# Kernel tuning notes

Measured on AMD Instinct MI355X. Metric: run time of the kernel, lower is better.

## Reference

```python
import jax, jax.numpy as jnp
import numpy as np

B, S, F, D, VOCAB, H = 1024, 512, 4, 32, 100001, 64
LN_EPS = 1e-3  # keras LayerNormalization default


def setup_inputs() -> dict:
    key = jax.random.key(0)
    ks = jax.random.split(key, 16)
    sd = 0.05
    return {
        "values": jax.random.normal(ks[0], (B, S, F), jnp.float32),
        "names": jax.random.randint(ks[1], (B, S), 0, VOCAB),
        "emb_table": jax.random.normal(ks[2], (VOCAB, D), jnp.float32) * sd,
        "W_num": jax.random.normal(ks[3], (F, D), jnp.float32) * sd,
        "b_num": jnp.zeros((D,), jnp.float32),
        "Wq": jax.random.normal(ks[4], (D, D), jnp.float32) * sd,
        "bq": jnp.zeros((D,), jnp.float32),
        "Wv": jax.random.normal(ks[5], (D, D), jnp.float32) * sd,
        "bv": jnp.zeros((D,), jnp.float32),
        "attn_scale": jnp.ones((D,), jnp.float32),
        "Wp": jax.random.normal(ks[6], (D, H), jnp.float32) * sd,
        "bp": jnp.zeros((H,), jnp.float32),
        "ln_gamma": jnp.ones((H,), jnp.float32),
        "ln_beta": jnp.zeros((H,), jnp.float32),
        "Ws": jax.random.normal(ks[7], (H, 2), jnp.float32) * sd,
    }


def reference(values, names, emb_table, W_num, b_num, Wq, bq, Wv, bv,
              attn_scale, Wp, bp, ln_gamma, ln_beta, Ws):
    # embeddings + numerical projection  [B,S,D]
    v = values @ W_num + b_num
    e = emb_table[names]
    mix = e + v
    # query from last position, value/key from the rest
    q = mix[:, -1:, :] @ Wq + bq          # [B,1,D]
    val = mix[:, :-1, :] @ Wv + bv        # [B,S-1,D]
    # keras AdditiveAttention (use_scale=True): score = sum(scale*tanh(q+k))
    scores = jnp.sum(attn_scale * jnp.tanh(q[:, :, None, :] + val[:, None, :, :]), axis=-1)  # [B,1,S-1]
    attn = jax.nn.softmax(scores, axis=-1)
    emb_out = jnp.einsum('bij,bjd->bid', attn, val)  # [B,1,D]
    # broadcast add then mean over sequence
    context = jnp.mean(emb_out + mix, axis=1)        # [B,D]
    # predictor: Dense(relu) + LayerNorm(axis=1 == features)
    h = jax.nn.relu(context @ Wp + bp)               # [B,H]
    mu = jnp.mean(h, axis=1, keepdims=True)
    var = jnp.var(h, axis=1, keepdims=True)
    h = (h - mu) * jax.lax.rsqrt(var + LN_EPS) * ln_gamma + ln_beta
    # scorer: Dense(2, softmax, no bias)
    score = jax.nn.softmax(h @ Ws, axis=-1)          # [B,2]
    return (score, emb_out, attn, h)
```

## Files before the change

kernel.cpp:

```cpp
#include <hip/hip_runtime.h>
#include <hip/hip_bf16.h>
#include <math.h>

constexpr int Bsz   = 1024;
constexpr int S     = 512;
constexpr int SV    = 511;
constexpr int D     = 32;
constexpr int F     = 4;
constexpr int H     = 64;
constexpr int BDIM  = 256;
constexpr int VOCAB = 100001;
constexpr size_t TAB_BYTES = (size_t)VOCAB * 64 * 2;

__device__ __forceinline__ float fast_tanh(float x) {
  const float ex = __expf(2.f * x);
  return 1.f - 2.f * __builtin_amdgcn_rcpf(ex + 1.f);
}

__device__ __forceinline__ void unpack8(uint4 u, float* f) {
  f[0] = __uint_as_float(u.x << 16); f[1] = __uint_as_float(u.x & 0xffff0000u);
  f[2] = __uint_as_float(u.y << 16); f[3] = __uint_as_float(u.y & 0xffff0000u);
  f[4] = __uint_as_float(u.z << 16); f[5] = __uint_as_float(u.z & 0xffff0000u);
  f[6] = __uint_as_float(u.w << 16); f[7] = __uint_as_float(u.w & 0xffff0000u);
}

__global__ __launch_bounds__(BDIM) void build_tab(
    const float* __restrict__ emb, const float* __restrict__ Wv,
    const float* __restrict__ W_num, const float* __restrict__ b_num,
    const float* __restrict__ bv,
    __hip_bfloat16* __restrict__ T, float* __restrict__ wsc)
{
  __shared__ float sWv[D * D];
  for (int i = threadIdx.x; i < D * D; i += BDIM) sWv[i] = Wv[i];
  __syncthreads();

  if (blockIdx.x == gridDim.x - 1) {
    const int tid = threadIdx.x;
    if (tid < F * D) {
      const int f = tid >> 5, k = tid & 31;
      float a = 0.f;
      #pragma unroll
      for (int m = 0; m < D; m++) a += W_num[f * D + m] * sWv[m * D + k];
      wsc[k * 4 + f] = a;
    } else if (tid < F * D + D) {
      const int k = tid - F * D;
      float a = bv[k];
      #pragma unroll
      for (int m = 0; m < D; m++) a += b_num[m] * sWv[m * D + k];
      wsc[F * D + k] = a;
    }
    return;
  }

  const int lr = threadIdx.x >> 5, k = threadIdx.x & 31;
  const int row = blockIdx.x * 8 + lr;
  if (row < VOCAB) {
    const float4* e4 = reinterpret_cast<const float4*>(emb + (size_t)row * D);
    float a = 0.f;
    #pragma unroll
    for (int c = 0; c < 8; c++) {
      const float4 v = e4[c];
      a += v.x * sWv[(4 * c + 0) * D + k] + v.y * sWv[(4 * c + 1) * D + k]
         + v.z * sWv[(4 * c + 2) * D + k] + v.w * sWv[(4 * c + 3) * D + k];
    }
    T[(size_t)row * 64 + k]      = __float2bfloat16(emb[(size_t)row * D + k]);
    T[(size_t)row * 64 + 32 + k] = __float2bfloat16(a);
  }
}

__global__ __launch_bounds__(BDIM, 4) void attn_main(
    const float* __restrict__ values, const int* __restrict__ names,
    const __hip_bfloat16* __restrict__ T, const float* __restrict__ wsc,
    const float* __restrict__ emb,
    const float* __restrict__ W_num, const float* __restrict__ b_num,
    const float* __restrict__ Wq,    const float* __restrict__ bq,
    const float* __restrict__ attn_scale,
    const float* __restrict__ Wp,    const float* __restrict__ bp,
    const float* __restrict__ ln_g,  const float* __restrict__ ln_b,
    const float* __restrict__ Ws,
    float* __restrict__ out_score, float* __restrict__ out_emb,
    float* __restrict__ out_attn,  float* __restrict__ out_h)
{
  __shared__ float sW2T[D][4];
  __shared__ float sQS[D][2];
  __shared__ float smixq[D];
  __shared__ float sred[4][69];
  __shared__ float sctx[D];
  __shared__ float sL[1];
  __shared__ float sE[512];

  const int b = blockIdx.x, tid = threadIdx.x, lane = tid & 63, wv = tid >> 6;
  const int rg = lane >> 2, kl = lane & 3;
  const int rbase = wv * 16 + rg;

  if (tid < 128) sW2T[tid >> 2][tid & 3] = wsc[tid];
  if (tid < D) {
    const int    nq = names[b * S + (S - 1)];
    const float* vr = values + (size_t)(b * S + (S - 1)) * F;
    smixq[tid] = emb[(size_t)nq * D + tid] + b_num[tid]
               + vr[0] * W_num[tid] + vr[1] * W_num[D + tid]
               + vr[2] * W_num[2 * D + tid] + vr[3] * W_num[3 * D + tid];
  }
  __syncthreads();
  if (tid < D) {
    float a = bq[tid];
    #pragma unroll
    for (int m = 0; m < D; m++) a += smixq[m] * Wq[m * D + tid];
    sQS[tid][0] = a + wsc[128 + tid];
    sQS[tid][1] = attn_scale[tid];
  }
  __syncthreads();

  float qb[8], scl[8], w2a[8], w2b[8], w2c[8], w2d[8];
  #pragma unroll
  for (int i = 0; i < 8; i++) {
    const int k = kl * 8 + i;
    qb[i]  = sQS[k][0]; scl[i] = sQS[k][1];
    w2a[i] = sW2T[k][0]; w2b[i] = sW2T[k][1];
    w2c[i] = sW2T[k][2]; w2d[i] = sW2T[k][3];
  }

  int nm[8];
  #pragma unroll
  for (int p = 0; p < 8; p++) nm[p] = names[b * S + p * 64 + rbase];

  float esum[8], acc[8];
  #pragma unroll
  for (int i = 0; i < 8; i++) { esum[i] = 0.f; acc[i] = 0.f; }
  float lloc = 0.f, vs0 = 0.f, vs1 = 0.f, vs2 = 0.f, vs3 = 0.f;

  const char* Tb = (const char*)T;
  uint4 Ec, Wc, En, Wn; float4 vc, vn;
  {
    const char* p0 = Tb + (size_t)nm[0] * 128 + kl * 16;
    Ec = *(const uint4*)p0; Wc = *(const uint4*)(p0 + 64);
    vc = *reinterpret_cast<const float4*>(values + (size_t)(b * S + rbase) * F);
    const char* p1 = Tb + (size_t)nm[1] * 128 + kl * 16;
    En = *(const uint4*)p1; Wn = *(const uint4*)(p1 + 64);
    vn = *reinterpret_cast<const float4*>(values + (size_t)(b * S + 64 + rbase) * F);
  }

  #pragma unroll
  for (int p = 0; p < 8; p++) {
    float em[8], w[8], t[8];
    unpack8(Ec, em); unpack8(Wc, w);
    float s = 0.f;
    #pragma unroll
    for (int i = 0; i < 8; i++) {
      t[i] = w[i] + qb[i] + vc.x * w2a[i] + vc.y * w2b[i]
           + vc.z * w2c[i] + vc.w * w2d[i];
      s += scl[i] * fast_tanh(t[i]);
    }
    const float4 vcur = vc;
    Ec = En; Wc = Wn; vc = vn;
    if (p + 2 < 8) {
      const char* pn = Tb + (size_t)nm[p + 2] * 128 + kl * 16;
      En = *(const uint4*)pn; Wn = *(const uint4*)(pn + 64);
      vn = *reinterpret_cast<const float4*>(values + (size_t)(b * S + (p + 2) * 64 + rbase) * F);
    }
    s += __shfl_xor(s, 1); s += __shfl_xor(s, 2);
    const bool  valid = (p * 64 + rbase) < SV;
    const float e = valid ? __expf(s) : 0.f;
    lloc += e;
    if (kl == 0) sE[p * 64 + rbase] = e;
    if (valid) {
      vs0 += vcur.x; vs1 += vcur.y; vs2 += vcur.z; vs3 += vcur.w;
      #pragma unroll
      for (int i = 0; i < 8; i++) esum[i] += em[i];
    }
    #pragma unroll
    for (int i = 0; i < 8; i++) acc[i] = fmaf(e, t[i], acc[i]);
  }

  #pragma unroll
  for (int off = 4; off < 64; off <<= 1) {
    lloc += __shfl_xor(lloc, off);
    vs0 += __shfl_xor(vs0, off); vs1 += __shfl_xor(vs1, off);
    vs2 += __shfl_xor(vs2, off); vs3 += __shfl_xor(vs3, off);
    #pragma unroll
    for (int i = 0; i < 8; i++) {
      acc[i]  += __shfl_xor(acc[i], off);
      esum[i] += __shfl_xor(esum[i], off);
    }
  }
  if (lane < 4) {
    #pragma unroll
    for (int i = 0; i < 8; i++) {
      sred[wv][lane * 8 + i]      = acc[i];
      sred[wv][32 + lane * 8 + i] = esum[i];
    }
  }
  if (lane == 0) {
    sred[wv][64] = lloc;
    sred[wv][65] = vs0; sred[wv][66] = vs1; sred[wv][67] = vs2; sred[wv][68] = vs3;
  }
  __syncthreads();
  if (tid == 0) sL[0] = sred[0][64] + sred[1][64] + sred[2][64] + sred[3][64];
  __syncthreads();
  const float invL = 1.f / sL[0];

  for (int idx = tid; idx < SV; idx += BDIM)
    out_attn[(size_t)b * SV + idx] = sE[idx] * invL;

  if (tid < D) {
    const float aS = sred[0][tid] + sred[1][tid] + sred[2][tid] + sred[3][tid];
    const float eS = sred[0][D + tid] + sred[1][D + tid] + sred[2][D + tid] + sred[3][D + tid];
    float vp = 0.f;
    #pragma unroll
    for (int f = 0; f < 4; f++) {
      const float vf = sred[0][65 + f] + sred[1][65 + f] + sred[2][65 + f] + sred[3][65 + f];
      vp += vf * W_num[f * D + tid];
    }
    const float q  = sQS[tid][0] - wsc[128 + tid];
    const float eo = aS * invL - q;
    out_emb[(size_t)b * D + tid] = eo;
    sctx[tid] = eo + (eS + vp + (float)SV * b_num[tid] + smixq[tid]) * (1.f / (float)S);
  }
  __syncthreads();

  if (tid < H) {
    float hv = bp[tid];
    #pragma unroll
    for (int d = 0; d < D; d++) hv += sctx[d] * Wp[d * H + tid];
    hv = fmaxf(hv, 0.f);
    float mu = hv;
    #pragma unroll
    for (int off = 32; off; off >>= 1) mu += __shfl_xor(mu, off);
    mu *= (1.f / 64.f);
    const float dv = hv - mu;
    float vvv = dv * dv;
    #pragma unroll
    for (int off = 32; off; off >>= 1) vvv += __shfl_xor(vvv, off);
    vvv *= (1.f / 64.f);
    const float hn = dv * rsqrtf(vvv + 1e-3f) * ln_g[tid] + ln_b[tid];
    out_h[(size_t)b * H + tid] = hn;
    float s0 = hn * Ws[2 * tid], s1 = hn * Ws[2 * tid + 1];
    #pragma unroll
    for (int off = 32; off; off >>= 1) { s0 += __shfl_xor(s0, off); s1 += __shfl_xor(s1, off); }
    if (tid == 0) {
      const float mx = fmaxf(s0, s1);
      const float a0 = __expf(s0 - mx), a1 = __expf(s1 - mx);
      const float inv = 1.f / (a0 + a1);
      out_score[(size_t)b * 2]     = a0 * inv;
      out_score[(size_t)b * 2 + 1] = a1 * inv;
    }
  }
}

__global__ __launch_bounds__(BDIM) void attn_fused_gemv(
    const float* __restrict__ values, const int* __restrict__ names,
    const float* __restrict__ emb,
    const float* __restrict__ W_num, const float* __restrict__ b_num,
    const float* __restrict__ Wq,    const float* __restrict__ bq,
    const float* __restrict__ Wv,    const float* __restrict__ bv,
    const float* __restrict__ attn_scale,
    const float* __restrict__ Wp,    const float* __restrict__ bp,
    const float* __restrict__ ln_g,  const float* __restrict__ ln_b,
    const float* __restrict__ Ws,
    float* __restrict__ out_score, float* __restrict__ out_emb,
    float* __restrict__ out_attn,  float* __restrict__ out_h)
{
  __shared__ float sWnum[F * D];
  __shared__ float sbnum[D];
  __shared__ float sWq[D * D];
  __shared__ float sWv[D * D];
  __shared__ float sbv[D];
  __shared__ float sscale[D];
  __shared__ float sq[D];
  __shared__ float smixq[D];
  __shared__ float sred[4][2 * D];
  __shared__ float sredS[4];
  __shared__ float sML[2];
  __shared__ float sctx[D];
  __shared__ float sWp[D * H];

  const int b = blockIdx.x, tid = threadIdx.x, lane = tid & 63, wv = tid >> 6;

  for (int i = tid; i < F * D; i += BDIM) sWnum[i] = W_num[i];
  if (tid < D) { sbnum[tid] = b_num[tid]; sbv[tid] = bv[tid]; sscale[tid] = attn_scale[tid]; }
  for (int i = tid; i < D * D; i += BDIM) { sWq[i] = Wq[i]; sWv[i] = Wv[i]; }
  for (int i = tid; i < D * H; i += BDIM) sWp[i] = Wp[i];
  __syncthreads();

  if (tid < D) {
    const int    name = names[b * S + (S - 1)];
    const float* vr   = values + (size_t)(b * S + (S - 1)) * F;
    smixq[tid] = emb[(size_t)name * D + tid] + sbnum[tid]
               + vr[0] * sWnum[tid] + vr[1] * sWnum[D + tid]
               + vr[2] * sWnum[2 * D + tid] + vr[3] * sWnum[3 * D + tid];
  }
  __syncthreads();
  if (tid < D) {
    float a = bq[tid];
    #pragma unroll
    for (int k = 0; k < D; k++) a += smixq[k] * sWq[k * D + tid];
    sq[tid] = a;
  }
  __syncthreads();

  float msum[D], acc[D];
  #pragma unroll
  for (int k = 0; k < D; k++) { msum[k] = 0.f; acc[k] = 0.f; }
  float mloc = -INFINITY, lloc = 0.f;
  float sc0 = 0.f, sc1 = 0.f;
  const bool has2 = (tid < SV - BDIM);

  auto row = [&](int j, float& sout) {
    const int    name = names[b * S + j];
    const float4 v4   = *reinterpret_cast<const float4*>(values + (size_t)(b * S + j) * F);
    const float4* e4p = reinterpret_cast<const float4*>(emb + (size_t)name * D);
    float mix[D];
    #pragma unroll
    for (int c = 0; c < 8; c++) {
      const float4 e = e4p[c];
      mix[4 * c] = e.x; mix[4 * c + 1] = e.y; mix[4 * c + 2] = e.z; mix[4 * c + 3] = e.w;
    }
    #pragma unroll
    for (int k = 0; k < D; k++) {
      mix[k] += sbnum[k] + v4.x * sWnum[k] + v4.y * sWnum[D + k]
              + v4.z * sWnum[2 * D + k] + v4.w * sWnum[3 * D + k];
      msum[k] += mix[k];
    }
    float val[D];
    #pragma unroll
    for (int k = 0; k < D; k++) val[k] = sbv[k];
    for (int m = 0; m < D; m++) {
      const float mv = mix[m];
      #pragma unroll
      for (int k = 0; k < D; k++) val[k] += mv * sWv[m * D + k];
    }
    float s = 0.f;
    #pragma unroll
    for (int k = 0; k < D; k++) s += sscale[k] * fast_tanh(sq[k] + val[k]);
    sout = s;
    float w;
    if (s > mloc) {
      const float sf = __expf(mloc - s);
      lloc *= sf;
      #pragma unroll
      for (int k = 0; k < D; k++) acc[k] *= sf;
      mloc = s; w = 1.f;
    } else {
      w = __expf(s - mloc);
    }
    lloc += w;
    #pragma unroll
    for (int k = 0; k < D; k++) acc[k] += w * val[k];
  };

  row(tid, sc0);
  if (has2) row(tid + BDIM, sc1);

  float mw = mloc;
  #pragma unroll
  for (int off = 32; off; off >>= 1) mw = fmaxf(mw, __shfl_xor(mw, off));
  if (lane == 0) sredS[wv] = mw;
  __syncthreads();
  if (tid == 0) sML[0] = fmaxf(fmaxf(sredS[0], sredS[1]), fmaxf(sredS[2], sredS[3]));
  __syncthreads();
  const float M = sML[0];
  {
    const float adj = __expf(mloc - M);
    lloc *= adj;
    #pragma unroll
    for (int k = 0; k < D; k++) acc[k] *= adj;
  }
  float lw = lloc;
  #pragma unroll
  for (int off = 32; off; off >>= 1) lw += __shfl_xor(lw, off);
  if (lane == 0) sredS[wv] = lw;
  #pragma unroll
  for (int k = 0; k < D; k++) {
    float a = acc[k], mm = msum[k];
    #pragma unroll
    for (int off = 32; off; off >>= 1) { a += __shfl_xor(a, off); mm += __shfl_xor(mm, off); }
    if (lane == 0) { sred[wv][k] = a; sred[wv][D + k] = mm; }
  }
  __syncthreads();
  if (tid == 0) sML[1] = sredS[0] + sredS[1] + sredS[2] + sredS[3];
  __syncthreads();
  const float L = sML[1], invL = 1.f / L;

  out_attn[(size_t)b * SV + tid] = __expf(sc0 - M) * invL;
  if (has2) out_attn[(size_t)b * SV + tid + BDIM] = __expf(sc1 - M) * invL;

  if (tid < D) {
    const float a  = sred[0][tid] + sred[1][tid] + sred[2][tid] + sred[3][tid];
    const float mm = sred[0][D + tid] + sred[1][D + tid] + sred[2][D + tid] + sred[3][D + tid];
    const float eo = a * invL;
    out_emb[(size_t)b * D + tid] = eo;
    sctx[tid] = eo + (mm + smixq[tid]) * (1.f / (float)S);
  }
  __syncthreads();

  if (tid < H) {
    float hv = bp[tid];
    #pragma unroll
    for (int d = 0; d < D; d++) hv += sctx[d] * sWp[d * H + tid];
    hv = fmaxf(hv, 0.f);
    float mu = hv;
    #pragma unroll
    for (int off = 32; off; off >>= 1) mu += __shfl_xor(mu, off);
    mu *= (1.f / 64.f);
    const float dv = hv - mu;
    float vv = dv * dv;
    #pragma unroll
    for (int off = 32; off; off >>= 1) vv += __shfl_xor(vv, off);
    vv *= (1.f / 64.f);
    const float hn = dv * rsqrtf(vv + 1e-3f) * ln_g[tid] + ln_b[tid];
    out_h[(size_t)b * H + tid] = hn;
    float s0 = hn * Ws[2 * tid], s1 = hn * Ws[2 * tid + 1];
    #pragma unroll
    for (int off = 32; off; off >>= 1) { s0 += __shfl_xor(s0, off); s1 += __shfl_xor(s1, off); }
    if (tid == 0) {
      const float mx = fmaxf(s0, s1);
      const float a0 = __expf(s0 - mx), a1 = __expf(s1 - mx);
      const float inv = 1.f / (a0 + a1);
      out_score[(size_t)b * 2]     = a0 * inv;
      out_score[(size_t)b * 2 + 1] = a1 * inv;
    }
  }
}

extern "C" void kernel_launch(void* const* d_in, const int* in_sizes, int n_in,
                              void* d_out, int out_size, void* d_ws, size_t ws_size,
                              hipStream_t stream) {
  const float* values = (const float*)d_in[0];
  const int*   names  = (const int*)d_in[1];
  const float* emb    = (const float*)d_in[2];
  const float* W_num  = (const float*)d_in[3];
  const float* b_num  = (const float*)d_in[4];
  const float* Wq     = (const float*)d_in[5];
  const float* bq     = (const float*)d_in[6];
  const float* Wv     = (const float*)d_in[7];
  const float* bv     = (const float*)d_in[8];
  const float* scal   = (const float*)d_in[9];
  const float* Wp     = (const float*)d_in[10];
  const float* bp     = (const float*)d_in[11];
  const float* ln_g   = (const float*)d_in[12];
  const float* ln_b   = (const float*)d_in[13];
  const float* Ws     = (const float*)d_in[14];

  float* out      = (float*)d_out;
  float* o_score  = out;
  float* o_emb    = o_score + (size_t)Bsz * 2;
  float* o_attn   = o_emb   + (size_t)Bsz * D;
  float* o_h      = o_attn  + (size_t)Bsz * SV;

  const size_t need = TAB_BYTES + 256 * sizeof(float);
  if (ws_size >= need) {
    __hip_bfloat16* T = (__hip_bfloat16*)d_ws;
    float* wsc = (float*)((char*)d_ws + TAB_BYTES);
    hipLaunchKernelGGL(build_tab, dim3((VOCAB + 7) / 8 + 1), dim3(BDIM), 0, stream,
                       emb, Wv, W_num, b_num, bv, T, wsc);
    hipLaunchKernelGGL(attn_main, dim3(Bsz), dim3(BDIM), 0, stream,
                       values, names, T, wsc, emb, W_num, b_num, Wq, bq, scal,
                       Wp, bp, ln_g, ln_b, Ws, o_score, o_emb, o_attn, o_h);
  } else {
    hipLaunchKernelGGL(attn_fused_gemv, dim3(Bsz), dim3(BDIM), 0, stream,
                       values, names, emb, W_num, b_num, Wq, bq, Wv, bv, scal,
                       Wp, bp, ln_g, ln_b, Ws, o_score, o_emb, o_attn, o_h);
  }
}
```

Baseline: 151.4 us.

## Remap attention threads to 8 lanes per row with deeper gather prefetch

Each table row is now split across 8 lanes with 4 features each instead of 4 lanes with 8, giving 16 iterations of 32 rows per block. Gathers use a 3-deep prefetch ring fed by names staged once in shared memory, and the minimum-blocks launch bound is dropped. The aim is more memory-level parallelism with fewer registers per thread, at the cost of narrower 8-byte loads and an extra shuffle step in each row reduction.

```diff
diff --git a/kernel.cpp b/kernel.cpp
--- a/kernel.cpp
+++ b/kernel.cpp
@@ -15,6 +15,11 @@
 __device__ __forceinline__ float fast_tanh(float x) {
   const float ex = __expf(2.f * x);
   return 1.f - 2.f * __builtin_amdgcn_rcpf(ex + 1.f);
+}
+
+__device__ __forceinline__ void unpack4(uint2 u, float* f) {
+  f[0] = __uint_as_float(u.x << 16); f[1] = __uint_as_float(u.x & 0xffff0000u);
+  f[2] = __uint_as_float(u.y << 16); f[3] = __uint_as_float(u.y & 0xffff0000u);
 }
 
 __device__ __forceinline__ void unpack8(uint4 u, float* f) {
@@ -68,7 +73,7 @@
   }
 }
 
-__global__ __launch_bounds__(BDIM, 4) void attn_main(
+__global__ __launch_bounds__(BDIM) void attn_main(
     const float* __restrict__ values, const int* __restrict__ names,
     const __hip_bfloat16* __restrict__ T, const float* __restrict__ wsc,
     const float* __restrict__ emb,
@@ -88,14 +93,16 @@
   __shared__ float sctx[D];
   __shared__ float sL[1];
   __shared__ float sE[512];
+  __shared__ int   sNames[512];
 
   const int b = blockIdx.x, tid = threadIdx.x, lane = tid & 63, wv = tid >> 6;
-  const int rg = lane >> 2, kl = lane & 3;
-  const int rbase = wv * 16 + rg;
-
+  const int kl = lane & 7, rg = lane >> 3;
+  const int rbase = wv * 8 + rg;
+
+  reinterpret_cast<int2*>(sNames)[tid] = *reinterpret_cast<const int2*>(names + (size_t)b * S + tid * 2);
   if (tid < 128) sW2T[tid >> 2][tid & 3] = wsc[tid];
   if (tid < D) {
-    const int    nq = names[b * S + (S - 1)];
+    const int    nq = names[(size_t)b * S + (S - 1)];
     const float* vr = values + (size_t)(b * S + (S - 1)) * F;
     smixq[tid] = emb[(size_t)nq * D + tid] + b_num[tid]
                + vr[0] * W_num[tid] + vr[1] * W_num[D + tid]
@@ -111,83 +118,77 @@
   }
   __syncthreads();
 
-  float qb[8], scl[8], w2a[8], w2b[8], w2c[8], w2d[8];
-  #pragma unroll
-  for (int i = 0; i < 8; i++) {
-    const int k = kl * 8 + i;
+  float qb[4], scl[4], w2a[4], w2b[4], w2c[4], w2d[4];
+  #pragma unroll
+  for (int i = 0; i < 4; i++) {
+    const int k = kl * 4 + i;
     qb[i]  = sQS[k][0]; scl[i] = sQS[k][1];
     w2a[i] = sW2T[k][0]; w2b[i] = sW2T[k][1];
     w2c[i] = sW2T[k][2]; w2d[i] = sW2T[k][3];
   }
 
-  int nm[8];
-  #pragma unroll
-  for (int p = 0; p < 8; p++) nm[p] = names[b * S + p * 64 + rbase];
-
-  float esum[8], acc[8];
-  #pragma unroll
-  for (int i = 0; i < 8; i++) { esum[i] = 0.f; acc[i] = 0.f; }
+  float esum[4] = {0.f, 0.f, 0.f, 0.f}, acc[4] = {0.f, 0.f, 0.f, 0.f};
   float lloc = 0.f, vs0 = 0.f, vs1 = 0.f, vs2 = 0.f, vs3 = 0.f;
 
   const char* Tb = (const char*)T;
-  uint4 Ec, Wc, En, Wn; float4 vc, vn;
-  {
-    const char* p0 = Tb + (size_t)nm[0] * 128 + kl * 16;
-    Ec = *(const uint4*)p0; Wc = *(const uint4*)(p0 + 64);
-    vc = *reinterpret_cast<const float4*>(values + (size_t)(b * S + rbase) * F);
-    const char* p1 = Tb + (size_t)nm[1] * 128 + kl * 16;
-    En = *(const uint4*)p1; Wn = *(const uint4*)(p1 + 64);
-    vn = *reinterpret_cast<const float4*>(values + (size_t)(b * S + 64 + rbase) * F);
-  }
-
-  #pragma unroll
-  for (int p = 0; p < 8; p++) {
-    float em[8], w[8], t[8];
-    unpack8(Ec, em); unpack8(Wc, w);
+  uint2 Eb[4], Wb[4]; float4 vb[4];
+
+  #define ISSUE(P, ST) do {                                                    \
+    const int   j_  = (P) * 32 + rbase;                                        \
+    const int   nm_ = sNames[j_];                                              \
+    const char* pr_ = Tb + (size_t)nm_ * 128 + kl * 8;                         \
+    Eb[ST] = *(const uint2*)pr_;                                               \
+    Wb[ST] = *(const uint2*)(pr_ + 64);                                        \
+    vb[ST] = *reinterpret_cast<const float4*>(values + (size_t)(b * S + j_) * F); \
+  } while (0)
+
+  ISSUE(0, 0); ISSUE(1, 1); ISSUE(2, 2);
+
+  #pragma unroll
+  for (int p = 0; p < 16; p++) {
+    const int st = p & 3;
+    float em[4], w[4], t[4];
+    unpack4(Eb[st], em); unpack4(Wb[st], w);
+    const float4 vv = vb[st];
+    if (p + 3 < 16) { const int sn = (p + 3) & 3; ISSUE(p + 3, sn); }
     float s = 0.f;
     #pragma unroll
-    for (int i = 0; i < 8; i++) {
-      t[i] = w[i] + qb[i] + vc.x * w2a[i] + vc.y * w2b[i]
-           + vc.z * w2c[i] + vc.w * w2d[i];
+    for (int i = 0; i < 4; i++) {
+      t[i] = w[i] + qb[i] + vv.x * w2a[i] + vv.y * w2b[i]
+           + vv.z * w2c[i] + vv.w * w2d[i];
       s += scl[i] * fast_tanh(t[i]);
     }
-    const float4 vcur = vc;
-    Ec = En; Wc = Wn; vc = vn;
-    if (p + 2 < 8) {
-      const char* pn = Tb + (size_t)nm[p + 2] * 128 + kl * 16;
-      En = *(const uint4*)pn; Wn = *(const uint4*)(pn + 64);
-      vn = *reinterpret_cast<const float4*>(values + (size_t)(b * S + (p + 2) * 64 + rbase) * F);
-    }
-    s += __shfl_xor(s, 1); s += __shfl_xor(s, 2);
-    const bool  valid = (p * 64 + rbase) < SV;
+    s += __shfl_xor(s, 1); s += __shfl_xor(s, 2); s += __shfl_xor(s, 4);
+    const bool  valid = (p * 32 + rbase) < SV;
     const float e = valid ? __expf(s) : 0.f;
     lloc += e;
-    if (kl == 0) sE[p * 64 + rbase] = e;
+    if (kl == 0) sE[p * 32 + rbase] = e;
     if (valid) {
-      vs0 += vcur.x; vs1 += vcur.y; vs2 += vcur.z; vs3 += vcur.w;
+      vs0 += vv.x; vs1 += vv.y; vs2 += vv.z; vs3 += vv.w;
       #pragma unroll
-      for (int i = 0; i < 8; i++) esum[i] += em[i];
-    }
-    #pragma unroll
-    for (int i = 0; i < 8; i++) acc[i] = fmaf(e, t[i], acc[i]);
-  }
-
-  #pragma unroll
-  for (int off = 4; off < 64; off <<= 1) {
+      for (int i = 0; i < 4; i++) esum[i] += em[i];
+    }
+    #pragma unroll
+    for (int i = 0; i < 4; i++) acc[i] = fmaf(e, t[i], acc[i]);
+  }
+  #undef ISSUE
+
+  #pragma unroll
+  for (int off = 8; off < 64; off <<= 1) {
     lloc += __shfl_xor(lloc, off);
     vs0 += __shfl_xor(vs0, off); vs1 += __shfl_xor(vs1, off);
     vs2 += __shfl_xor(vs2, off); vs3 += __shfl_xor(vs3, off);
     #pragma unroll
-    for (int i = 0; i < 8; i++) {
+    for (int i = 0; i < 4; i++) {
       acc[i]  += __shfl_xor(acc[i], off);
       esum[i] += __shfl_xor(esum[i], off);
     }
   }
-  if (lane < 4) {
-    #pragma unroll
-    for (int i = 0; i < 8; i++) {
-      sred[wv][lane * 8 + i]      = acc[i];
-      sred[wv][32 + lane * 8 + i] = esum[i];
+  if (lane < 8) {
+    #pragma unroll
+    for (int i = 0; i < 4; i++) {
+      sred[wv][lane * 4 + i]      = acc[i];
+      sred[wv][32 + lane * 4 + i] = esum[i];
     }
   }
   if (lane == 0) {
```

Measured after the change: 132.6 us. 1.14x faster.
